# Performance work log

Measured on AMD Instinct MI355X. Metric: run time of the kernel, lower is better.

## Reference

```python
import jax, jax.numpy as jnp
import numpy as np

NUM_RBF = 16
MAX_REL = 32          # max_relative_feature
AUTOREGRESSIVE = True
D_MIN, D_MAX = 2.0, 22.0
LN_EPS = 1e-5


def setup_inputs() -> dict:
    key = jax.random.key(0)
    ks = jax.random.split(key, 6)
    B, L, A, K = 1, 1280, 14, 30
    E_feat, edge_in = 128, 16 + NUM_RBF * 4 * 10  # 656
    X = jax.random.normal(ks[0], (B, L, A, 3), dtype=jnp.float32) * 3.0
    residue_idx = jnp.tile(jnp.arange(L, dtype=jnp.int32)[None], (B, 1))
    chain_labels = jnp.zeros((B, L), dtype=jnp.int32)
    E_idx = jax.random.randint(ks[1], (B, L, K), 0, L, dtype=jnp.int32)
    atom_mask = jnp.ones((B, L, A), dtype=jnp.float32)
    W_pos = jax.random.normal(ks[2], (2 * MAX_REL + 2, 16), dtype=jnp.float32) * 0.1
    b_pos = jnp.zeros((16,), dtype=jnp.float32)
    W_edge = jax.random.normal(ks[3], (edge_in, E_feat), dtype=jnp.float32) * 0.05
    ln_gamma = jnp.ones((E_feat,), dtype=jnp.float32)
    ln_beta = jnp.zeros((E_feat,), dtype=jnp.float32)
    return {"X": X, "residue_idx": residue_idx, "chain_labels": chain_labels,
            "E_idx": E_idx, "atom_mask": atom_mask, "W_pos": W_pos,
            "b_pos": b_pos, "W_edge": W_edge, "ln_gamma": ln_gamma,
            "ln_beta": ln_beta}


def _forward(X, residue_idx, chain_labels, E_idx, W_pos, b_pos, W_edge,
             ln_gamma, ln_beta):
    B, L, A, _ = X.shape
    K = E_idx.shape[-1]
    # backbone atoms in loop order [Ca, N, C, O] -> X indices [1, 0, 2, 3]
    bb = X[:, :, jnp.array([1, 0, 2, 3]), :]          # [B, L, 4, 3]
    sc = X[:, :, 4:, :]                               # [B, L, 10, 3]
    Abb = jnp.transpose(bb, (0, 2, 1, 3))             # [B, 4, L, 3]
    Asc = jnp.transpose(sc, (0, 2, 1, 3))             # [B, 10, L, 3]
    # dense pairwise distances for all 40 (bb, sc) atom pairs: [B,4,10,L,L]
    diff = Abb[:, :, None, :, None, :] - Asc[:, None, :, None, :, :]
    D = jnp.sqrt(jnp.sum(diff * diff, axis=-1) + 1e-6)
    # gather top-k neighbor columns -> [B,4,10,L,K]
    D_nb = jnp.take_along_axis(D, E_idx[:, None, None, :, :], axis=4)
    mu = jnp.linspace(D_MIN, D_MAX, NUM_RBF, dtype=D_nb.dtype)
    sigma = (D_MAX - D_MIN) / NUM_RBF
    RBF = jnp.exp(-(((D_nb[..., None] - mu) / sigma) ** 2))  # [B,4,10,L,K,16]
    if AUTOREGRESSIVE:
        self_edges = (E_idx == jnp.arange(L, dtype=E_idx.dtype)[None, :, None])
        RBF = jnp.where(self_edges[:, None, None, :, :, None], 0.0, RBF)
    # concat order: bb outer, sc inner -> [B,L,K, 4*10*16]
    RBF_all = jnp.transpose(RBF, (0, 3, 4, 1, 2, 5)).reshape(B, L, K, 4 * 10 * NUM_RBF)
    # positional encodings
    offset = residue_idx[:, :, None] - residue_idx[:, None, :]        # [B,L,L]
    offset = jnp.take_along_axis(offset, E_idx, axis=2)               # [B,L,K]
    d_chains = (chain_labels[:, :, None] == chain_labels[:, None, :]).astype(jnp.int32)
    E_chains = jnp.take_along_axis(d_chains, E_idx, axis=2)           # [B,L,K]
    d = jnp.clip(offset + MAX_REL, 0, 2 * MAX_REL) * E_chains + (1 - E_chains) * (2 * MAX_REL + 1)
    d_onehot = jax.nn.one_hot(d, 2 * MAX_REL + 2, dtype=W_pos.dtype)  # [B,L,K,66]
    E_positional = d_onehot @ W_pos + b_pos                           # [B,L,K,16]
    E = jnp.concatenate([E_positional, RBF_all], axis=-1)             # [B,L,K,656]
    E = E @ W_edge                                                    # no bias
    # LayerNorm over last dim
    mean = jnp.mean(E, axis=-1, keepdims=True)
    var = jnp.mean((E - mean) ** 2, axis=-1, keepdims=True)
    E = (E - mean) / jnp.sqrt(var + LN_EPS) * ln_gamma + ln_beta
    return E


def reference(X, residue_idx, chain_labels, E_idx, atom_mask, W_pos, b_pos,
              W_edge, ln_gamma, ln_beta):
    E = _forward(X, residue_idx, chain_labels, E_idx, W_pos, b_pos, W_edge,
                 ln_gamma, ln_beta)
    return (E, E_idx)
```

## Files before the change

### kernel.cpp

```cpp
#include <hip/hip_runtime.h>

typedef short bf16x8 __attribute__((ext_vector_type(8)));
typedef float f32x4  __attribute__((ext_vector_type(4)));

#define L_RES 1280
#define A_ATM 14
#define K_NB  30
#define FEAT  656
#define KPAD  672
#define NCH   128
#define AF_STRIDE 680
#define E_OUT_OFF (L_RES * K_NB * NCH)

__device__ __forceinline__ ushort f2bf(float x) {
    union { float f; unsigned u; } v; v.f = x;
    unsigned r = (v.u + 0x7fffu + ((v.u >> 16) & 1u)) >> 16;
    return (ushort)r;
}

__global__ __launch_bounds__(256) void wt_convert_kernel(const float* __restrict__ W,
                                                         ushort* __restrict__ Wt) {
    int idx = blockIdx.x * 256 + threadIdx.x;
    if (idx >= NCH * KPAD) return;
    int n = idx / KPAD, k = idx - n * KPAD;
    float v = (k < FEAT) ? W[k * NCH + n] : 0.0f;
    Wt[idx] = f2bf(v);
}

__global__ __launch_bounds__(256) void sidechain_feat_kernel(
    const float* __restrict__ X,
    const int*   __restrict__ ridx,
    const int*   __restrict__ clab,
    const int*   __restrict__ Eidx,
    const float* __restrict__ Wpos,
    const float* __restrict__ bpos,
    const ushort* __restrict__ Wt,
    const float* __restrict__ gamma,
    const float* __restrict__ beta,
    float* __restrict__ out)
{
    __shared__ __align__(16) ushort Af[32][AF_STRIDE];
    __shared__ float bbs[4][3];
    __shared__ float scj[K_NB][10][3];
    __shared__ int   nbr[K_NB];

    const int i = blockIdx.x;
    const int t = threadIdx.x;
    const int w = t >> 6;
    const int lane = t & 63;

    if (t < 12) {
        const int perm[4] = {1, 0, 2, 3};
        int a = t / 3, c = t - a * 3;
        bbs[a][c] = X[(i * A_ATM + perm[a]) * 3 + c];
    }
    if (t < K_NB) nbr[t] = Eidx[i * K_NB + t];
    __syncthreads();

    for (int idx = t; idx < K_NB * 30; idx += 256) {
        int e = idx / 30;
        int r = idx - e * 30;
        int a = r / 3, c = r - a * 3;
        scj[e][a][c] = X[(nbr[e] * A_ATM + 4 + a) * 3 + c];
    }

    for (int idx = t; idx < K_NB * 16; idx += 256) {
        int e = idx >> 4, c = idx & 15;
        int j = nbr[e];
        int d;
        if (clab[i] == clab[j]) {
            int off = ridx[i] - ridx[j] + 32;
            d = off < 0 ? 0 : (off > 64 ? 64 : off);
        } else {
            d = 65;
        }
        Af[e][c] = f2bf(Wpos[d * 16 + c] + bpos[c]);
    }
    for (int idx = t; idx < 2 * AF_STRIDE; idx += 256)
        Af[30 + idx / AF_STRIDE][idx % AF_STRIDE] = 0;
    for (int idx = t; idx < 30 * 24; idx += 256)
        Af[idx / 24][FEAT + idx % 24] = 0;
    __syncthreads();

    for (int idx = t; idx < K_NB * 40; idx += 256) {
        int e  = idx / 40;
        int p  = idx - e * 40;
        int ab = p / 10, as = p - ab * 10;
        float dx = bbs[ab][0] - scj[e][as][0];
        float dy = bbs[ab][1] - scj[e][as][1];
        float dz = bbs[ab][2] - scj[e][as][2];
        float dist = sqrtf(dx * dx + dy * dy + dz * dz + 1e-6f);
        bool self = (nbr[e] == i);
        unsigned* dst = (unsigned*)&Af[e][16 + p * 16];
#pragma unroll
        for (int q = 0; q < 8; q++) {
            float m0 = 2.0f + (float)(2 * q)     * (20.0f / 15.0f);
            float m1 = 2.0f + (float)(2 * q + 1) * (20.0f / 15.0f);
            float a0 = (dist - m0) * 0.8f;
            float a1 = (dist - m1) * 0.8f;
            float r0 = self ? 0.0f : __expf(-a0 * a0);
            float r1 = self ? 0.0f : __expf(-a1 * a1);
            dst[q] = (unsigned)f2bf(r0) | ((unsigned)f2bf(r1) << 16);
        }
    }
    __syncthreads();

    const int frow = lane & 15;
    const int quad = lane >> 4;
    const ushort* A0p = &Af[frow][quad * 8];
    const ushort* A1p = &Af[16 + frow][quad * 8];
    const ushort* B0p = Wt + (size_t)((2 * w) * 16 + frow) * KPAD + quad * 8;
    const ushort* B1p = B0p + 16 * KPAD;

    f32x4 acc00 = {0.f,0.f,0.f,0.f}, acc01 = {0.f,0.f,0.f,0.f};
    f32x4 acc10 = {0.f,0.f,0.f,0.f}, acc11 = {0.f,0.f,0.f,0.f};

    bf16x8 a0 = *(const bf16x8*)(A0p);
    bf16x8 a1 = *(const bf16x8*)(A1p);
    bf16x8 b0 = *(const bf16x8*)(B0p);
    bf16x8 b1 = *(const bf16x8*)(B1p);

#pragma unroll
    for (int kb = 0; kb < KPAD; kb += 32) {
        bf16x8 ca0 = a0, ca1 = a1, cb0 = b0, cb1 = b1;
        if (kb + 32 < KPAD) {
            a0 = *(const bf16x8*)(A0p + kb + 32);
            a1 = *(const bf16x8*)(A1p + kb + 32);
            b0 = *(const bf16x8*)(B0p + kb + 32);
            b1 = *(const bf16x8*)(B1p + kb + 32);
        }
        acc00 = __builtin_amdgcn_mfma_f32_16x16x32_bf16(ca0, cb0, acc00, 0, 0, 0);
        acc01 = __builtin_amdgcn_mfma_f32_16x16x32_bf16(ca0, cb1, acc01, 0, 0, 0);
        acc10 = __builtin_amdgcn_mfma_f32_16x16x32_bf16(ca1, cb0, acc10, 0, 0, 0);
        acc11 = __builtin_amdgcn_mfma_f32_16x16x32_bf16(ca1, cb1, acc11, 0, 0, 0);
    }

    __syncthreads();
    float (*Epre)[132] = (float (*)[132])&Af[0][0];

#pragma unroll
    for (int r = 0; r < 4; r++) {
        int row0 = quad * 4 + r;
        Epre[row0][(2 * w)     * 16 + frow] = acc00[r];
        Epre[row0][(2 * w + 1) * 16 + frow] = acc01[r];
        Epre[16 + row0][(2 * w)     * 16 + frow] = acc10[r];
        Epre[16 + row0][(2 * w + 1) * 16 + frow] = acc11[r];
    }
    __syncthreads();

    for (int e = w; e < K_NB; e += 4) {
        float v0 = Epre[e][lane];
        float v1 = Epre[e][lane + 64];
        float s = v0 + v1;
        float q = v0 * v0 + v1 * v1;
#pragma unroll
        for (int off = 32; off > 0; off >>= 1) {
            s += __shfl_xor(s, off);
            q += __shfl_xor(q, off);
        }
        float mean = s * (1.0f / 128.0f);
        float var  = q * (1.0f / 128.0f) - mean * mean;
        float rstd = rsqrtf(var + 1e-5f);
        float* o = out + (size_t)(i * K_NB + e) * NCH;
        o[lane]      = (v0 - mean) * rstd * gamma[lane]      + beta[lane];
        o[lane + 64] = (v1 - mean) * rstd * gamma[lane + 64] + beta[lane + 64];
    }

    if (t < K_NB) out[E_OUT_OFF + i * K_NB + t] = (float)nbr[t];
}

extern "C" void kernel_launch(void* const* d_in, const int* in_sizes, int n_in,
                              void* d_out, int out_size, void* d_ws, size_t ws_size,
                              hipStream_t stream) {
    const float* X     = (const float*)d_in[0];
    const int*   ridx  = (const int*)  d_in[1];
    const int*   clab  = (const int*)  d_in[2];
    const int*   Eidx  = (const int*)  d_in[3];
    const float* Wpos  = (const float*)d_in[5];
    const float* bpos  = (const float*)d_in[6];
    const float* Wedge = (const float*)d_in[7];
    const float* gamma = (const float*)d_in[8];
    const float* beta  = (const float*)d_in[9];
    float* out = (float*)d_out;

    ushort* Wt = (ushort*)d_ws;

    wt_convert_kernel<<<(NCH * KPAD + 255) / 256, 256, 0, stream>>>(Wedge, Wt);
    sidechain_feat_kernel<<<L_RES, 256, 0, stream>>>(
        X, ridx, clab, Eidx, Wpos, bpos, Wt, gamma, beta, out);
}
```

Before: 108.9 us.

## Fuse weight fp32-to-bf16 conversion into main kernel via per-chunk LDS staging

Removes the separate weight transpose/convert kernel. Each wave now loads its fp32 W_edge slice per 32-wide K chunk, converts it to bf16 and stores it transposed into a small LDS scratch buffer that is shared with the sidechain coordinate staging. That buffer then feeds the MFMA. It also adds an occupancy hint to launch bounds. The trade-off is one fewer launch and a leaner LDS footprint in exchange for every block redoing the weight conversion. The B tile is written and read by the same wave with no barrier between chunks, so correctness depends on ordering within a single wave.

```diff
diff --git a/kernel.cpp b/kernel.cpp
--- a/kernel.cpp
+++ b/kernel.cpp
@@ -7,9 +7,10 @@
 #define A_ATM 14
 #define K_NB  30
 #define FEAT  656
-#define KPAD  672
 #define NCH   128
 #define AF_STRIDE 680
+#define BT_STRIDE 40
+#define SCRATCH_BYTES (NCH * BT_STRIDE * 2)
 #define E_OUT_OFF (L_RES * K_NB * NCH)
 
 __device__ __forceinline__ ushort f2bf(float x) {
@@ -18,31 +19,26 @@
     return (ushort)r;
 }
 
-__global__ __launch_bounds__(256) void wt_convert_kernel(const float* __restrict__ W,
-                                                         ushort* __restrict__ Wt) {
-    int idx = blockIdx.x * 256 + threadIdx.x;
-    if (idx >= NCH * KPAD) return;
-    int n = idx / KPAD, k = idx - n * KPAD;
-    float v = (k < FEAT) ? W[k * NCH + n] : 0.0f;
-    Wt[idx] = f2bf(v);
-}
-
-__global__ __launch_bounds__(256) void sidechain_feat_kernel(
+__global__ __launch_bounds__(256, 3) void sidechain_feat_kernel(
     const float* __restrict__ X,
     const int*   __restrict__ ridx,
     const int*   __restrict__ clab,
     const int*   __restrict__ Eidx,
     const float* __restrict__ Wpos,
     const float* __restrict__ bpos,
-    const ushort* __restrict__ Wt,
+    const float* __restrict__ Wedge,
     const float* __restrict__ gamma,
     const float* __restrict__ beta,
     float* __restrict__ out)
 {
     __shared__ __align__(16) ushort Af[32][AF_STRIDE];
+    __shared__ __align__(16) unsigned char scratch[SCRATCH_BYTES];
     __shared__ float bbs[4][3];
-    __shared__ float scj[K_NB][10][3];
     __shared__ int   nbr[K_NB];
+
+    float  (*scj)[10][3]    = reinterpret_cast<float (*)[10][3]>(scratch);
+    ushort (*Bt)[BT_STRIDE] = reinterpret_cast<ushort (*)[BT_STRIDE]>(scratch);
+    unsigned* BtW           = reinterpret_cast<unsigned*>(scratch);
 
     const int i = blockIdx.x;
     const int t = threadIdx.x;
@@ -109,30 +105,52 @@
     const int quad = lane >> 4;
     const ushort* A0p = &Af[frow][quad * 8];
     const ushort* A1p = &Af[16 + frow][quad * 8];
-    const ushort* B0p = Wt + (size_t)((2 * w) * 16 + frow) * KPAD + quad * 8;
-    const ushort* B1p = B0p + 16 * KPAD;
+    const ushort* B0p = &Bt[32 * w + frow][quad * 8];
+    const ushort* B1p = &Bt[32 * w + 16 + frow][quad * 8];
+
+    const int ngrp  = lane & 7;
+    const int kpair = lane >> 3;
+    const int colw  = 32 * w + ngrp * 4;
 
     f32x4 acc00 = {0.f,0.f,0.f,0.f}, acc01 = {0.f,0.f,0.f,0.f};
     f32x4 acc10 = {0.f,0.f,0.f,0.f}, acc11 = {0.f,0.f,0.f,0.f};
 
-    bf16x8 a0 = *(const bf16x8*)(A0p);
-    bf16x8 a1 = *(const bf16x8*)(A1p);
-    bf16x8 b0 = *(const bf16x8*)(B0p);
-    bf16x8 b1 = *(const bf16x8*)(B1p);
-
-#pragma unroll
-    for (int kb = 0; kb < KPAD; kb += 32) {
-        bf16x8 ca0 = a0, ca1 = a1, cb0 = b0, cb1 = b1;
-        if (kb + 32 < KPAD) {
-            a0 = *(const bf16x8*)(A0p + kb + 32);
-            a1 = *(const bf16x8*)(A1p + kb + 32);
-            b0 = *(const bf16x8*)(B0p + kb + 32);
-            b1 = *(const bf16x8*)(B1p + kb + 32);
-        }
-        acc00 = __builtin_amdgcn_mfma_f32_16x16x32_bf16(ca0, cb0, acc00, 0, 0, 0);
-        acc01 = __builtin_amdgcn_mfma_f32_16x16x32_bf16(ca0, cb1, acc01, 0, 0, 0);
-        acc10 = __builtin_amdgcn_mfma_f32_16x16x32_bf16(ca1, cb0, acc10, 0, 0, 0);
-        acc11 = __builtin_amdgcn_mfma_f32_16x16x32_bf16(ca1, cb1, acc11, 0, 0, 0);
+    auto loadW = [&](f32x4* buf, int c) {
+        const int kb = c * 32 + kpair * 2;
+        const f32x4 z = {0.f,0.f,0.f,0.f};
+#pragma unroll
+        for (int r = 0; r < 2; ++r) {
+            int k = kb + r * 16;
+            buf[2*r+0] = (k     < FEAT) ? *(const f32x4*)(Wedge + k * NCH + colw)       : z;
+            buf[2*r+1] = (k + 1 < FEAT) ? *(const f32x4*)(Wedge + (k + 1) * NCH + colw) : z;
+        }
+    };
+    auto storeBt = [&](const f32x4* buf) {
+#pragma unroll
+        for (int r = 0; r < 2; ++r)
+#pragma unroll
+            for (int j = 0; j < 4; ++j) {
+                unsigned lo = f2bf(buf[2*r+0][j]);
+                unsigned hi = f2bf(buf[2*r+1][j]);
+                BtW[(colw + j) * (BT_STRIDE / 2) + r * 8 + kpair] = lo | (hi << 16);
+            }
+    };
+
+    f32x4 wcur[4], wnxt[4] = {};
+    loadW(wcur, 0);
+    for (int c = 0; c < 21; ++c) {
+        if (c + 1 < 21) loadW(wnxt, c + 1);
+        storeBt(wcur);
+        bf16x8 a0 = *(const bf16x8*)(A0p + c * 32);
+        bf16x8 a1 = *(const bf16x8*)(A1p + c * 32);
+        bf16x8 b0 = *(const bf16x8*)(B0p);
+        bf16x8 b1 = *(const bf16x8*)(B1p);
+        acc00 = __builtin_amdgcn_mfma_f32_16x16x32_bf16(a0, b0, acc00, 0, 0, 0);
+        acc01 = __builtin_amdgcn_mfma_f32_16x16x32_bf16(a0, b1, acc01, 0, 0, 0);
+        acc10 = __builtin_amdgcn_mfma_f32_16x16x32_bf16(a1, b0, acc10, 0, 0, 0);
+        acc11 = __builtin_amdgcn_mfma_f32_16x16x32_bf16(a1, b1, acc11, 0, 0, 0);
+#pragma unroll
+        for (int q = 0; q < 4; ++q) wcur[q] = wnxt[q];
     }
 
     __syncthreads();
@@ -183,9 +201,8 @@
     const float* beta  = (const float*)d_in[9];
     float* out = (float*)d_out;
 
-    ushort* Wt = (ushort*)d_ws;
-
-    wt_convert_kernel<<<(NCH * KPAD + 255) / 256, 256, 0, stream>>>(Wedge, Wt);
+    (void)d_ws; (void)ws_size;
+
     sidechain_feat_kernel<<<L_RES, 256, 0, stream>>>(
-        X, ridx, clab, Eidx, Wpos, bpos, Wt, gamma, beta, out);
+        X, ridx, clab, Eidx, Wpos, bpos, Wedge, gamma, beta, out);
 }
```

Result: slower. 127.6 us (+17.2%).

## Fuse LayerNorm into MFMA epilogue, prefetch weights early, drop smem staging passes

Applied to the files above, without the earlier changes.

LayerNorm statistics are now reduced directly from the MFMA accumulators using shuffles plus a small shared partial-sum array, instead of spilling the full pre-norm tile to shared memory and re-reading it. The weight fragments and gamma/beta are loaded before the feature phase, and B loads use a two-step prefetch. The side-chain coordinate staging buffer, its barrier and the zeroing of the padding rows are removed; features are built in unrolled loops with a packed bf16 convert instruction. Launch bounds now request 3 blocks per CU. Risks: output stores become 16-float segments per row rather than full-row coalesced writes, and the unused padding rows of the A tile are left uninitialized.

```diff
diff --git a/kernel.cpp b/kernel.cpp
--- a/kernel.cpp
+++ b/kernel.cpp
@@ -27,7 +27,7 @@
     Wt[idx] = f2bf(v);
 }
 
-__global__ __launch_bounds__(256) void sidechain_feat_kernel(
+__global__ __launch_bounds__(256, 3) void sidechain_feat_kernel(
     const float* __restrict__ X,
     const int*   __restrict__ ridx,
     const int*   __restrict__ clab,
@@ -41,13 +41,26 @@
 {
     __shared__ __align__(16) ushort Af[32][AF_STRIDE];
     __shared__ float bbs[4][3];
-    __shared__ float scj[K_NB][10][3];
     __shared__ int   nbr[K_NB];
+    __shared__ __align__(16) float part[32][4][2];
 
     const int i = blockIdx.x;
     const int t = threadIdx.x;
     const int w = t >> 6;
     const int lane = t & 63;
+    const int frow = lane & 15;
+    const int quad = lane >> 4;
+    const int c0 = (2 * w) * 16 + frow;
+    const int c1 = c0 + 16;
+
+    const ushort* B0p = Wt + (size_t)c0 * KPAD + quad * 8;
+    const ushort* B1p = Wt + (size_t)c1 * KPAD + quad * 8;
+    bf16x8 b0c = *(const bf16x8*)(B0p);
+    bf16x8 b1c = *(const bf16x8*)(B1p);
+    bf16x8 b0n = *(const bf16x8*)(B0p + 32);
+    bf16x8 b1n = *(const bf16x8*)(B1p + 32);
+    float gg0 = gamma[c0], gg1 = gamma[c1];
+    float be0 = beta[c0],  be1 = beta[c1];
 
     if (t < 12) {
         const int perm[4] = {1, 0, 2, 3};
@@ -57,113 +70,143 @@
     if (t < K_NB) nbr[t] = Eidx[i * K_NB + t];
     __syncthreads();
 
-    for (int idx = t; idx < K_NB * 30; idx += 256) {
-        int e = idx / 30;
-        int r = idx - e * 30;
-        int a = r / 3, c = r - a * 3;
-        scj[e][a][c] = X[(nbr[e] * A_ATM + 4 + a) * 3 + c];
-    }
-
-    for (int idx = t; idx < K_NB * 16; idx += 256) {
-        int e = idx >> 4, c = idx & 15;
-        int j = nbr[e];
-        int d;
-        if (clab[i] == clab[j]) {
-            int off = ridx[i] - ridx[j] + 32;
-            d = off < 0 ? 0 : (off > 64 ? 64 : off);
-        } else {
-            d = 65;
-        }
-        Af[e][c] = f2bf(Wpos[d * 16 + c] + bpos[c]);
-    }
-    for (int idx = t; idx < 2 * AF_STRIDE; idx += 256)
-        Af[30 + idx / AF_STRIDE][idx % AF_STRIDE] = 0;
-    for (int idx = t; idx < 30 * 24; idx += 256)
-        Af[idx / 24][FEAT + idx % 24] = 0;
+    const int my_clab = clab[i];
+    const int my_ridx = ridx[i];
+
+#pragma unroll
+    for (int u = 0; u < 2; ++u) {
+        int idx = t + u * 256;
+        if (idx < K_NB * 16) {
+            int e = idx >> 4, c = idx & 15;
+            int j = nbr[e];
+            int d;
+            if (my_clab == clab[j]) {
+                int off = my_ridx - ridx[j] + 32;
+                d = off < 0 ? 0 : (off > 64 ? 64 : off);
+            } else {
+                d = 65;
+            }
+            Af[e][c] = f2bf(Wpos[d * 16 + c] + bpos[c]);
+        }
+    }
+#pragma unroll
+    for (int u = 0; u < 2; ++u) {
+        int k = t + u * 256;
+        if (k < K_NB * 16) Af[k >> 4][FEAT + (k & 15)] = 0;
+    }
+#pragma unroll
+    for (int u = 0; u < 5; ++u) {
+        int idx = t + u * 256;
+        if (idx < K_NB * 40) {
+            int e  = idx / 40;
+            int p  = idx - e * 40;
+            int ab = p / 10, as = p - ab * 10;
+            int j = nbr[e];
+            const float* xp = X + (size_t)(j * A_ATM + 4 + as) * 3;
+            float dx = bbs[ab][0] - xp[0];
+            float dy = bbs[ab][1] - xp[1];
+            float dz = bbs[ab][2] - xp[2];
+            float dist = sqrtf(dx * dx + dy * dy + dz * dz + 1e-6f);
+            bool self = (j == i);
+            unsigned* dst = (unsigned*)&Af[e][16 + p * 16];
+#pragma unroll
+            for (int q = 0; q < 8; ++q) {
+                float m0 = 2.0f + (float)(2 * q)     * (20.0f / 15.0f);
+                float m1 = 2.0f + (float)(2 * q + 1) * (20.0f / 15.0f);
+                float a0 = (dist - m0) * 0.8f;
+                float a1 = (dist - m1) * 0.8f;
+                float r0 = self ? 0.0f : __expf(-a0 * a0);
+                float r1 = self ? 0.0f : __expf(-a1 * a1);
+                unsigned pk;
+                asm("v_cvt_pk_bf16_f32 %0, %1, %2" : "=v"(pk) : "v"(r0), "v"(r1));
+                dst[q] = pk;
+            }
+        }
+    }
     __syncthreads();
 
-    for (int idx = t; idx < K_NB * 40; idx += 256) {
-        int e  = idx / 40;
-        int p  = idx - e * 40;
-        int ab = p / 10, as = p - ab * 10;
-        float dx = bbs[ab][0] - scj[e][as][0];
-        float dy = bbs[ab][1] - scj[e][as][1];
-        float dz = bbs[ab][2] - scj[e][as][2];
-        float dist = sqrtf(dx * dx + dy * dy + dz * dz + 1e-6f);
-        bool self = (nbr[e] == i);
-        unsigned* dst = (unsigned*)&Af[e][16 + p * 16];
-#pragma unroll
-        for (int q = 0; q < 8; q++) {
-            float m0 = 2.0f + (float)(2 * q)     * (20.0f / 15.0f);
-            float m1 = 2.0f + (float)(2 * q + 1) * (20.0f / 15.0f);
-            float a0 = (dist - m0) * 0.8f;
-            float a1 = (dist - m1) * 0.8f;
-            float r0 = self ? 0.0f : __expf(-a0 * a0);
-            float r1 = self ? 0.0f : __expf(-a1 * a1);
-            dst[q] = (unsigned)f2bf(r0) | ((unsigned)f2bf(r1) << 16);
-        }
-    }
-    __syncthreads();
-
-    const int frow = lane & 15;
-    const int quad = lane >> 4;
     const ushort* A0p = &Af[frow][quad * 8];
     const ushort* A1p = &Af[16 + frow][quad * 8];
-    const ushort* B0p = Wt + (size_t)((2 * w) * 16 + frow) * KPAD + quad * 8;
-    const ushort* B1p = B0p + 16 * KPAD;
+    bf16x8 a0c = *(const bf16x8*)(A0p);
+    bf16x8 a1c = *(const bf16x8*)(A1p);
 
     f32x4 acc00 = {0.f,0.f,0.f,0.f}, acc01 = {0.f,0.f,0.f,0.f};
     f32x4 acc10 = {0.f,0.f,0.f,0.f}, acc11 = {0.f,0.f,0.f,0.f};
 
-    bf16x8 a0 = *(const bf16x8*)(A0p);
-    bf16x8 a1 = *(const bf16x8*)(A1p);
-    bf16x8 b0 = *(const bf16x8*)(B0p);
-    bf16x8 b1 = *(const bf16x8*)(B1p);
-
-#pragma unroll
-    for (int kb = 0; kb < KPAD; kb += 32) {
-        bf16x8 ca0 = a0, ca1 = a1, cb0 = b0, cb1 = b1;
-        if (kb + 32 < KPAD) {
-            a0 = *(const bf16x8*)(A0p + kb + 32);
-            a1 = *(const bf16x8*)(A1p + kb + 32);
-            b0 = *(const bf16x8*)(B0p + kb + 32);
-            b1 = *(const bf16x8*)(B1p + kb + 32);
-        }
-        acc00 = __builtin_amdgcn_mfma_f32_16x16x32_bf16(ca0, cb0, acc00, 0, 0, 0);
-        acc01 = __builtin_amdgcn_mfma_f32_16x16x32_bf16(ca0, cb1, acc01, 0, 0, 0);
-        acc10 = __builtin_amdgcn_mfma_f32_16x16x32_bf16(ca1, cb0, acc10, 0, 0, 0);
-        acc11 = __builtin_amdgcn_mfma_f32_16x16x32_bf16(ca1, cb1, acc11, 0, 0, 0);
-    }
-
+#pragma unroll
+    for (int c = 0; c < 21; ++c) {
+        bf16x8 ua0 = a0c, ua1 = a1c, ub0 = b0c, ub1 = b1c;
+        if (c + 1 < 21) {
+            a0c = *(const bf16x8*)(A0p + (c + 1) * 32);
+            a1c = *(const bf16x8*)(A1p + (c + 1) * 32);
+        }
+        b0c = b0n; b1c = b1n;
+        if (c + 2 < 21) {
+            b0n = *(const bf16x8*)(B0p + (c + 2) * 32);
+            b1n = *(const bf16x8*)(B1p + (c + 2) * 32);
+        }
+        acc00 = __builtin_amdgcn_mfma_f32_16x16x32_bf16(ua0, ub0, acc00, 0, 0, 0);
+        acc01 = __builtin_amdgcn_mfma_f32_16x16x32_bf16(ua0, ub1, acc01, 0, 0, 0);
+        acc10 = __builtin_amdgcn_mfma_f32_16x16x32_bf16(ua1, ub0, acc10, 0, 0, 0);
+        acc11 = __builtin_amdgcn_mfma_f32_16x16x32_bf16(ua1, ub1, acc11, 0, 0, 0);
+    }
+
+    float s0[4], q0[4], s1[4], q1[4];
+#pragma unroll
+    for (int r = 0; r < 4; ++r) {
+        s0[r] = acc00[r] + acc01[r];
+        q0[r] = acc00[r] * acc00[r] + acc01[r] * acc01[r];
+        s1[r] = acc10[r] + acc11[r];
+        q1[r] = acc10[r] * acc10[r] + acc11[r] * acc11[r];
+    }
+#pragma unroll
+    for (int off = 1; off < 16; off <<= 1) {
+#pragma unroll
+        for (int r = 0; r < 4; ++r) {
+            s0[r] += __shfl_xor(s0[r], off);
+            q0[r] += __shfl_xor(q0[r], off);
+            s1[r] += __shfl_xor(s1[r], off);
+            q1[r] += __shfl_xor(q1[r], off);
+        }
+    }
+    if (frow == 0) {
+#pragma unroll
+        for (int r = 0; r < 4; ++r) {
+            int row = quad * 4 + r;
+            part[row][w][0]      = s0[r];
+            part[row][w][1]      = q0[r];
+            part[16 + row][w][0] = s1[r];
+            part[16 + row][w][1] = q1[r];
+        }
+    }
     __syncthreads();
-    float (*Epre)[132] = (float (*)[132])&Af[0][0];
-
-#pragma unroll
-    for (int r = 0; r < 4; r++) {
-        int row0 = quad * 4 + r;
-        Epre[row0][(2 * w)     * 16 + frow] = acc00[r];
-        Epre[row0][(2 * w + 1) * 16 + frow] = acc01[r];
-        Epre[16 + row0][(2 * w)     * 16 + frow] = acc10[r];
-        Epre[16 + row0][(2 * w + 1) * 16 + frow] = acc11[r];
-    }
-    __syncthreads();
-
-    for (int e = w; e < K_NB; e += 4) {
-        float v0 = Epre[e][lane];
-        float v1 = Epre[e][lane + 64];
-        float s = v0 + v1;
-        float q = v0 * v0 + v1 * v1;
-#pragma unroll
-        for (int off = 32; off > 0; off >>= 1) {
-            s += __shfl_xor(s, off);
-            q += __shfl_xor(q, off);
-        }
-        float mean = s * (1.0f / 128.0f);
-        float var  = q * (1.0f / 128.0f) - mean * mean;
-        float rstd = rsqrtf(var + 1e-5f);
-        float* o = out + (size_t)(i * K_NB + e) * NCH;
-        o[lane]      = (v0 - mean) * rstd * gamma[lane]      + beta[lane];
-        o[lane + 64] = (v1 - mean) * rstd * gamma[lane + 64] + beta[lane + 64];
+
+#pragma unroll
+    for (int r = 0; r < 4; ++r) {
+        int row = quad * 4 + r;
+        {
+            f32x4 pa = *(const f32x4*)&part[row][0][0];
+            f32x4 pb = *(const f32x4*)&part[row][2][0];
+            float S = pa[0] + pa[2] + pb[0] + pb[2];
+            float Q = pa[1] + pa[3] + pb[1] + pb[3];
+            float mean = S * (1.0f / 128.0f);
+            float rstd = rsqrtf(Q * (1.0f / 128.0f) - mean * mean + 1e-5f);
+            float* o = out + (size_t)(i * K_NB + row) * NCH;
+            o[c0] = (acc00[r] - mean) * rstd * gg0 + be0;
+            o[c1] = (acc01[r] - mean) * rstd * gg1 + be1;
+        }
+        int row1 = 16 + row;
+        if (row1 < K_NB) {
+            f32x4 pa = *(const f32x4*)&part[row1][0][0];
+            f32x4 pb = *(const f32x4*)&part[row1][2][0];
+            float S = pa[0] + pa[2] + pb[0] + pb[2];
+            float Q = pa[1] + pa[3] + pb[1] + pb[3];
+            float mean = S * (1.0f / 128.0f);
+            float rstd = rsqrtf(Q * (1.0f / 128.0f) - mean * mean + 1e-5f);
+            float* o = out + (size_t)(i * K_NB + row1) * NCH;
+            o[c0] = (acc10[r] - mean) * rstd * gg0 + be0;
+            o[c1] = (acc11[r] - mean) * rstd * gg1 + be1;
+        }
     }
 
     if (t < K_NB) out[E_OUT_OFF + i * K_NB + t] = (float)nbr[t];
```

New measurement: 103.7 us. -4.7%, faster.
